# Kernel optimization log

Hardware: AMD Instinct MI355X
Metric: run time of the kernel (lower is better)

## Reference

```python
import jax, jax.numpy as jnp
import numpy as np

C = 256
DQK = C // 8


def setup_inputs() -> dict:
    key = jax.random.key(0)
    ks = jax.random.split(key, 7)
    B, H, W = 8, 64, 64
    x = jax.random.normal(ks[0], (B, H, W, C), dtype=jnp.float32)
    # 1x1 conv weights (equivalent to per-pixel dense): [Cin, Cout] + bias
    sq = 1.0 / np.sqrt(C)
    Wq = jax.random.normal(ks[1], (C, DQK), dtype=jnp.float32) * sq
    bq = jnp.zeros((DQK,), dtype=jnp.float32)
    Wk = jax.random.normal(ks[2], (C, DQK), dtype=jnp.float32) * sq
    bk = jnp.zeros((DQK,), dtype=jnp.float32)
    Wv = jax.random.normal(ks[3], (C, C), dtype=jnp.float32) * sq
    bv = jnp.zeros((C,), dtype=jnp.float32)
    gamma = jnp.float32(0.5)  # nonzero so attention path affects output/grads
    return {"x": x, "Wq": Wq, "bq": bq, "Wk": Wk, "bk": bk,
            "Wv": Wv, "bv": bv, "gamma": gamma}


def reference(x, Wq, bq, Wk, bk, Wv, bv, gamma):
    B, H, W, c = x.shape
    n = H * W
    xf = x.reshape(B, n, c)                      # [B, hw, C]
    q = xf @ Wq + bq                              # [B, hw, C//8]
    k = xf @ Wk + bk                              # [B, hw, C//8]
    v = xf @ Wv + bv                              # [B, hw, C]
    scores = jnp.einsum('bnd,bmd->bnm', q, k)     # [B, hw, hw], no scaling (faithful)
    attn = jax.nn.softmax(scores, axis=-1)
    out = jnp.einsum('bnm,bmc->bnc', attn, v)     # [B, hw, C]
    out = out.reshape(B, H, W, c)
    return gamma * out + x
```

## Files before the change

kernel.cpp:

```cpp
#include <hip/hip_runtime.h>
#include <hip/hip_bf16.h>
#include <math.h>

#define B_ 8
#define N_ 4096
#define C_ 256
#define DQK_ 32

typedef float f32x4  __attribute__((ext_vector_type(4)));
typedef float f32x16 __attribute__((ext_vector_type(16)));
typedef short bf16x8 __attribute__((ext_vector_type(8)));
typedef short bf16x4 __attribute__((ext_vector_type(4)));

__device__ __forceinline__ short f2bf(float f){
  union { float f; unsigned u; } v; v.f = f;
  unsigned r = v.u + 0x7fffu + ((v.u >> 16) & 1u);
  return (short)(r >> 16);
}

__global__ void cast_wt_kernel(const float* __restrict__ Wq, const float* __restrict__ Wk,
                               const float* __restrict__ Wv, short* __restrict__ WT){
  int n = blockIdx.x;
  int k = threadIdx.x;
  float val;
  if (n < 32)       val = Wq[k*32 + n];
  else if (n < 64)  val = Wk[k*32 + (n-32)];
  else              val = Wv[k*256 + (n-64)];
  WT[n*256 + k] = f2bf(val);
}

__global__ __launch_bounds__(256) void proj_kernel(
    const float* __restrict__ x, const short* __restrict__ WT,
    const float* __restrict__ bq, const float* __restrict__ bk, const float* __restrict__ bv,
    short* __restrict__ qws, short* __restrict__ kws, short* __restrict__ vSw){
  __shared__ __align__(16) short sX[64*264];
  __shared__ __align__(16) short sT[64*72];
  int tid = threadIdx.x;
  int lane = tid & 63, wave = tid >> 6;
  int lane15 = lane & 15, quad = lane >> 4;
  int mbase = blockIdx.x * 64;
  int b = mbase >> 12, kvb = mbase & (N_-1);

  const float* xr = x + (size_t)mbase * C_;
  for (int i = 0; i < 8; i++){
    int s = tid + i*256;
    int row = s >> 5, cg = (s & 31) << 3;
    const f32x4* src = (const f32x4*)(xr + row*C_ + cg);
    f32x4 a = src[0], c = src[1];
    bf16x8 p;
    p[0]=f2bf(a[0]); p[1]=f2bf(a[1]); p[2]=f2bf(a[2]); p[3]=f2bf(a[3]);
    p[4]=f2bf(c[0]); p[5]=f2bf(c[1]); p[6]=f2bf(c[2]); p[7]=f2bf(c[3]);
    *(bf16x8*)(sX + row*264 + cg) = p;
  }
  __syncthreads();

  f32x4 acc[5][4];
  for (int i=0;i<5;i++) for (int mt=0;mt<4;mt++) acc[i][mt] = (f32x4)(0.f);

  for (int kc = 0; kc < 8; kc++){
    bf16x8 afr[4];
    #pragma unroll
    for (int mt=0;mt<4;mt++)
      afr[mt] = *(const bf16x8*)(sX + (mt*16+lane15)*264 + kc*32 + quad*8);
    bf16x8 bfr[5];
    #pragma unroll
    for (int i=0;i<5;i++){
      int t = i*4 + wave;
      bfr[i] = *(const bf16x8*)(WT + (size_t)(t*16+lane15)*256 + kc*32 + quad*8);
    }
    #pragma unroll
    for (int i=0;i<5;i++)
      #pragma unroll
      for (int mt=0;mt<4;mt++)
        acc[i][mt] = __builtin_amdgcn_mfma_f32_16x16x32_bf16(afr[mt], bfr[i], acc[i][mt], 0,0,0);
  }

  #pragma unroll
  for (int i=0;i<5;i++){
    int t = i*4 + wave;
    int n0 = t*16 + lane15;
    float bias = (n0 < 32) ? bq[n0] : (n0 < 64 ? bk[n0-32] : bv[n0-64]);
    if (n0 < 64){
      #pragma unroll
      for (int mt=0;mt<4;mt++)
        #pragma unroll
        for (int r=0;r<4;r++)
          sT[(mt*16 + quad*4 + r)*72 + n0] = f2bf(acc[i][mt][r] + bias);
    } else {
      int ch = n0 - 64, cht = ch >> 5, c5 = ch & 31;
      int lanep = c5 | ((quad & 1) << 5);
      int jo = (quad >> 1) * 4;
      #pragma unroll
      for (int mt=0;mt<4;mt++){
        bf16x4 pk;
        pk[0]=f2bf(acc[i][mt][0]+bias); pk[1]=f2bf(acc[i][mt][1]+bias);
        pk[2]=f2bf(acc[i][mt][2]+bias); pk[3]=f2bf(acc[i][mt][3]+bias);
        size_t off = (size_t)b*1048576 + (size_t)(kvb>>6)*16384
                   + (size_t)(mt*8 + cht)*512 + (size_t)lanep*8 + jo;
        *(bf16x4*)(vSw + off) = pk;
      }
    }
  }
  __syncthreads();

  {
    int qt = tid >> 7, p = (tid >> 6) & 1, ln = tid & 63;
    int row = qt*32 + (ln & 31);
    int dcol = p*16 + (ln >> 5)*8;
    bf16x8 vq = *(const bf16x8*)(sT + row*72 + dcol);
    bf16x8 vk = *(const bf16x8*)(sT + row*72 + 32 + dcol);
    size_t qoff = ((((size_t)b*128 + ((kvb>>5) + qt))*2 + p)*64 + ln)*8;
    *(bf16x8*)(qws + qoff) = vq;
    size_t koff = ((size_t)b*64 + (kvb>>6))*2048 + (size_t)((qt*2 + p)*64 + ln)*8;
    *(bf16x8*)(kws + koff) = vk;
  }
}

__global__ __launch_bounds__(512, 2) void flash_kernel(
    const float* __restrict__ x, const short* __restrict__ qws, const short* __restrict__ kws,
    const short* __restrict__ vSw, const float* __restrict__ gptr, float* __restrict__ out){
  __shared__ __align__(16) char smem[131072];
  int tid = threadIdx.x;
  int lane = tid & 63, wave = tid >> 6;
  int l31 = lane & 31, h = lane >> 5;
  int qt = wave >> 1, kh = wave & 1;
  int b = blockIdx.x & 7;
  int q0 = (blockIdx.x >> 3) << 7;

  const short* qb = qws + (size_t)b*131072;
  const short* kb = kws + (size_t)b*131072;
  const short* vb = vSw + (size_t)b*1048576;

  int qtg = (q0 >> 5) + qt;
  bf16x8 qf0 = *(const bf16x8*)(qb + (size_t)((qtg*2+0)*64 + lane)*8);
  bf16x8 qf1 = *(const bf16x8*)(qb + (size_t)((qtg*2+1)*64 + lane)*8);

  const short* kf0p = kb + (size_t)((2*kh+0)*64 + lane)*8;
  const short* kf1p = kb + (size_t)((2*kh+1)*64 + lane)*8;

#define VPREF(CHUNK, DST) do { \
    const short* vsrc_ = vb + (size_t)(CHUNK)*16384; \
    _Pragma("unroll") \
    for (int r_=0;r_<4;r_++) \
      __builtin_amdgcn_global_load_lds( \
        (const __attribute__((address_space(1))) void*)(vsrc_ + (size_t)(r_*512+tid)*8), \
        (__attribute__((address_space(3))) void*)((DST) + (size_t)(r_*512+tid)*8), 16, 0, 0); \
  } while(0)

  VPREF(0, (short*)smem);
  VPREF(1, (short*)(smem + 32768));
  __builtin_amdgcn_sched_barrier(0);
  bf16x8 kfc0 = *(const bf16x8*)(kf0p);
  bf16x8 kfc1 = *(const bf16x8*)(kf1p);
  __builtin_amdgcn_sched_barrier(0);
  bf16x8 kfn0, kfn1;

  f32x16 acc[8];
  #pragma unroll
  for (int t=0;t<8;t++) acc[t] = (f32x16)(0.f);
  float rsO = 0.f;

  for (int it=0; it<64; it++){
    int nk = (it+1 < 64) ? (it+1) : 63;
    int ns = (it+2 < 64) ? (it+2) : 63;

    kfn0 = *(const bf16x8*)(kf0p + (size_t)nk*2048);
    kfn1 = *(const bf16x8*)(kf1p + (size_t)nk*2048);
    __builtin_amdgcn_sched_barrier(0);
    VPREF(ns, (short*)(smem + ((size_t)((it+2)&3))*32768));
    __builtin_amdgcn_sched_barrier(0);

    f32x16 s = __builtin_amdgcn_mfma_f32_32x32x16_bf16(kfc0, qf0, (f32x16)(0.f), 0,0,0);
    s        = __builtin_amdgcn_mfma_f32_32x32x16_bf16(kfc1, qf1, s, 0,0,0);
    bf16x8 pf[2];
    #pragma unroll
    for (int g=0; g<2; g++){
      union { bf16x8 v; unsigned u[4]; } P;
      #pragma unroll
      for (int j=0;j<4;j++){
        float2 e;
        e.x = __expf(s[g*8 + 2*j]);
        e.y = __expf(s[g*8 + 2*j + 1]);
        rsO += e.x + e.y;
        __hip_bfloat162 t2 = __float22bfloat162_rn(e);
        __builtin_memcpy(&P.u[j], &t2, 4);
      }
      pf[g] = P.v;
    }

    asm volatile("s_waitcnt vmcnt(4)" ::: "memory");
    __builtin_amdgcn_sched_barrier(0);
    __builtin_amdgcn_s_barrier();
    __builtin_amdgcn_sched_barrier(0);

    {
      const short* sVc = (const short*)(smem + ((size_t)(it&3))*32768);
      #pragma unroll
      for (int g=0; g<2; g++){
        const short* base = sVc + (2*kh + g)*4096;
        #pragma unroll
        for (int cht=0; cht<8; cht++){
          bf16x8 vf = *(const bf16x8*)(base + (cht*64 + lane)*8);
          acc[cht] = __builtin_amdgcn_mfma_f32_32x32x16_bf16(pf[g], vf, acc[cht], 0,0,0);
        }
      }
    }
    kfc0 = kfn0; kfc1 = kfn1;
  }

  asm volatile("s_waitcnt vmcnt(0)" ::: "memory");
  __builtin_amdgcn_sched_barrier(0);
  __builtin_amdgcn_s_barrier();
  __builtin_amdgcn_sched_barrier(0);

  rsO += __shfl_xor(rsO, 32);
  float* R1 = (float*)smem;
  float* RS = (float*)(smem + 65536);
  int pw = wave ^ 1;
  if (lane < 32) RS[wave*32 + l31] = rsO;

  if (kh == 0){
    #pragma unroll
    for (int i=0;i<16;i++){ R1[wave*2048 + i*64 + lane] = acc[4][i];
                            R1[wave*2048 + 1024 + i*64 + lane] = acc[5][i]; }
  } else {
    #pragma unroll
    for (int i=0;i<16;i++){ R1[wave*2048 + i*64 + lane] = acc[0][i];
                            R1[wave*2048 + 1024 + i*64 + lane] = acc[1][i]; }
  }
  __syncthreads();
  if (kh == 0){
    #pragma unroll
    for (int i=0;i<16;i++){ acc[0][i] += R1[pw*2048 + i*64 + lane];
                            acc[1][i] += R1[pw*2048 + 1024 + i*64 + lane]; }
  } else {
    #pragma unroll
    for (int i=0;i<16;i++){ acc[4][i] += R1[pw*2048 + i*64 + lane];
                            acc[5][i] += R1[pw*2048 + 1024 + i*64 + lane]; }
  }
  __syncthreads();
  if (kh == 0){
    #pragma unroll
    for (int i=0;i<16;i++){ R1[wave*2048 + i*64 + lane] = acc[6][i];
                            R1[wave*2048 + 1024 + i*64 + lane] = acc[7][i]; }
  } else {
    #pragma unroll
    for (int i=0;i<16;i++){ R1[wave*2048 + i*64 + lane] = acc[2][i];
                            R1[wave*2048 + 1024 + i*64 + lane] = acc[3][i]; }
  }
  __syncthreads();
  if (kh == 0){
    #pragma unroll
    for (int i=0;i<16;i++){ acc[2][i] += R1[pw*2048 + i*64 + lane];
                            acc[3][i] += R1[pw*2048 + 1024 + i*64 + lane]; }
  } else {
    #pragma unroll
    for (int i=0;i<16;i++){ acc[6][i] += R1[pw*2048 + i*64 + lane];
                            acc[7][i] += R1[pw*2048 + 1024 + i*64 + lane]; }
  }

  float g = *gptr;
  const float* xb = x + ((size_t)b*N_ + q0 + qt*32)*C_;
  float*       ob = out + ((size_t)b*N_ + q0 + qt*32)*C_;
  if (kh == 0){
    #pragma unroll
    for (int i=0;i<16;i++){
      int q = (i&3) + 8*(i>>2) + 4*h;
      float rv = 1.f / (RS[(qt*2+0)*32 + q] + RS[(qt*2+1)*32 + q]);
      #pragma unroll
      for (int ct=0; ct<4; ct++){
        int ch = ct*32 + l31;
        ob[(size_t)q*C_ + ch] = g*(acc[ct][i]*rv) + xb[(size_t)q*C_ + ch];
      }
    }
  } else {
    #pragma unroll
    for (int i=0;i<16;i++){
      int q = (i&3) + 8*(i>>2) + 4*h;
      float rv = 1.f / (RS[(qt*2+0)*32 + q] + RS[(qt*2+1)*32 + q]);
      #pragma unroll
      for (int ct=0; ct<4; ct++){
        int ch = (4+ct)*32 + l31;
        ob[(size_t)q*C_ + ch] = g*(acc[4+ct][i]*rv) + xb[(size_t)q*C_ + ch];
      }
    }
  }
#undef VPREF
}

extern "C" void kernel_launch(void* const* d_in, const int* in_sizes, int n_in,
                              void* d_out, int out_size, void* d_ws, size_t ws_size,
                              hipStream_t stream){
  const float* x  = (const float*)d_in[0];
  const float* Wq = (const float*)d_in[1];
  const float* bq = (const float*)d_in[2];
  const float* Wk = (const float*)d_in[3];
  const float* bk = (const float*)d_in[4];
  const float* Wv = (const float*)d_in[5];
  const float* bv = (const float*)d_in[6];
  const float* gm = (const float*)d_in[7];
  float* out = (float*)d_out;
  char* ws = (char*)d_ws;
  short* WT  = (short*)ws;
  short* qws = (short*)(ws + 163840);
  short* kws = (short*)(ws + 163840 + 2097152);
  short* vSw = (short*)(ws + 163840 + 2*2097152);

  cast_wt_kernel<<<dim3(320), dim3(256), 0, stream>>>(Wq, Wk, Wv, WT);
  proj_kernel<<<dim3(512), dim3(256), 0, stream>>>(x, WT, bq, bk, bv, qws, kws, vSw);
  flash_kernel<<<dim3(256), dim3(512), 0, stream>>>(x, qws, kws, vSw, gm, out);
}
```

Measured before the change: 194.4 us.

## Load V fragments directly from global memory instead of staging through LDS

Removes the 4-stage LDS ring buffer that V chunks were streamed into with global_load_lds, along with the per-iteration waitcnt and workgroup barrier. Each wave now loads its V fragments straight from global memory into registers right before the PV MFMAs, and LDS shrinks to what the epilogue reduction needs. The goals are to drop block-wide synchronisation and lower LDS use so more blocks can be resident. The cost is that global-load latency now sits directly before the MFMAs with no prefetch across iterations, and V traffic relies on L2 reuse rather than shared staging.

```diff
diff --git a/kernel.cpp b/kernel.cpp
--- a/kernel.cpp
+++ b/kernel.cpp
@@ -119,7 +119,7 @@
 __global__ __launch_bounds__(512, 2) void flash_kernel(
     const float* __restrict__ x, const short* __restrict__ qws, const short* __restrict__ kws,
     const short* __restrict__ vSw, const float* __restrict__ gptr, float* __restrict__ out){
-  __shared__ __align__(16) char smem[131072];
+  __shared__ __align__(16) char smem[66560];
   int tid = threadIdx.x;
   int lane = tid & 63, wave = tid >> 6;
   int l31 = lane & 31, h = lane >> 5;
@@ -137,23 +137,10 @@
 
   const short* kf0p = kb + (size_t)((2*kh+0)*64 + lane)*8;
   const short* kf1p = kb + (size_t)((2*kh+1)*64 + lane)*8;
-
-#define VPREF(CHUNK, DST) do { \
-    const short* vsrc_ = vb + (size_t)(CHUNK)*16384; \
-    _Pragma("unroll") \
-    for (int r_=0;r_<4;r_++) \
-      __builtin_amdgcn_global_load_lds( \
-        (const __attribute__((address_space(1))) void*)(vsrc_ + (size_t)(r_*512+tid)*8), \
-        (__attribute__((address_space(3))) void*)((DST) + (size_t)(r_*512+tid)*8), 16, 0, 0); \
-  } while(0)
-
-  VPREF(0, (short*)smem);
-  VPREF(1, (short*)(smem + 32768));
-  __builtin_amdgcn_sched_barrier(0);
   bf16x8 kfc0 = *(const bf16x8*)(kf0p);
   bf16x8 kfc1 = *(const bf16x8*)(kf1p);
-  __builtin_amdgcn_sched_barrier(0);
-  bf16x8 kfn0, kfn1;
+
+  const short* vlane = vb + (size_t)(2*kh)*4096 + (size_t)lane*8;
 
   f32x16 acc[8];
   #pragma unroll
@@ -161,17 +148,15 @@
   float rsO = 0.f;
 
   for (int it=0; it<64; it++){
-    int nk = (it+1 < 64) ? (it+1) : 63;
-    int ns = (it+2 < 64) ? (it+2) : 63;
-
-    kfn0 = *(const bf16x8*)(kf0p + (size_t)nk*2048);
-    kfn1 = *(const bf16x8*)(kf1p + (size_t)nk*2048);
-    __builtin_amdgcn_sched_barrier(0);
-    VPREF(ns, (short*)(smem + ((size_t)((it+2)&3))*32768));
-    __builtin_amdgcn_sched_barrier(0);
+    bf16x8 kfn0, kfn1;
+    if (it < 63){
+      kfn0 = *(const bf16x8*)(kf0p + (size_t)(it+1)*2048);
+      kfn1 = *(const bf16x8*)(kf1p + (size_t)(it+1)*2048);
+    }
 
     f32x16 s = __builtin_amdgcn_mfma_f32_32x32x16_bf16(kfc0, qf0, (f32x16)(0.f), 0,0,0);
     s        = __builtin_amdgcn_mfma_f32_32x32x16_bf16(kfc1, qf1, s, 0,0,0);
+
     bf16x8 pf[2];
     #pragma unroll
     for (int g=0; g<2; g++){
@@ -188,30 +173,20 @@
       pf[g] = P.v;
     }
 
-    asm volatile("s_waitcnt vmcnt(4)" ::: "memory");
-    __builtin_amdgcn_sched_barrier(0);
-    __builtin_amdgcn_s_barrier();
-    __builtin_amdgcn_sched_barrier(0);
-
-    {
-      const short* sVc = (const short*)(smem + ((size_t)(it&3))*32768);
-      #pragma unroll
-      for (int g=0; g<2; g++){
-        const short* base = sVc + (2*kh + g)*4096;
-        #pragma unroll
-        for (int cht=0; cht<8; cht++){
-          bf16x8 vf = *(const bf16x8*)(base + (cht*64 + lane)*8);
-          acc[cht] = __builtin_amdgcn_mfma_f32_32x32x16_bf16(pf[g], vf, acc[cht], 0,0,0);
-        }
-      }
-    }
-    kfc0 = kfn0; kfc1 = kfn1;
-  }
-
-  asm volatile("s_waitcnt vmcnt(0)" ::: "memory");
-  __builtin_amdgcn_sched_barrier(0);
-  __builtin_amdgcn_s_barrier();
-  __builtin_amdgcn_sched_barrier(0);
+    const short* vc = vlane + (size_t)it*16384;
+    #pragma unroll
+    for (int g=0; g<2; g++){
+      const short* base = vc + g*4096;
+      bf16x8 vf[8];
+      #pragma unroll
+      for (int c=0;c<8;c++) vf[c] = *(const bf16x8*)(base + c*512);
+      #pragma unroll
+      for (int c=0;c<8;c++)
+        acc[c] = __builtin_amdgcn_mfma_f32_32x32x16_bf16(pf[g], vf[c], acc[c], 0,0,0);
+    }
+
+    if (it < 63){ kfc0 = kfn0; kfc1 = kfn1; }
+  }
 
   rsO += __shfl_xor(rsO, 32);
   float* R1 = (float*)smem;
@@ -285,7 +260,6 @@
       }
     }
   }
-#undef VPREF
 }
 
 extern "C" void kernel_launch(void* const* d_in, const int* in_sizes, int n_in,
```

Result: slower. 203.3 us (+4.6%).
